# Optimization experiments

Measured on AMD Instinct MI355X. Metric: run time of the kernel, lower is better.

## Reference

```python
import jax, jax.numpy as jnp
import numpy as np

EPS = 1e-6

def _phi(x):
    # ELU + 1 feature map: strictly positive
    return jax.nn.elu(x) + 1.0

def setup_inputs() -> dict:
    key = jax.random.key(0)
    kq, kk, kv = jax.random.split(key, 3)
    B, T, H, D = 4, 8192, 16, 64
    q = jax.random.normal(kq, (B, T, H, D), dtype=jnp.float32)
    k = jax.random.normal(kk, (B, T, H, D), dtype=jnp.float32)
    v = jax.random.normal(kv, (B, T, H, D), dtype=jnp.float32)
    return {"q": q, "k": k, "v": v}

def _linear_attention(q, k, v):
    # q,k,v: [B,T,H,D] -> out [B,T,H,D]
    phi_q = _phi(q)
    phi_k = _phi(k)
    # time-major for scan: [T,B,H,D]
    pq = jnp.moveaxis(phi_q, 1, 0)
    pk = jnp.moveaxis(phi_k, 1, 0)
    vv = jnp.moveaxis(v, 1, 0)
    B, H, D = pq.shape[1], pq.shape[2], pq.shape[3]
    S0 = jnp.zeros((B, H, D, D), dtype=q.dtype)
    z0 = jnp.zeros((B, H, D), dtype=q.dtype)

    def step(carry, inp):
        S, z = carry
        q_t, k_t, v_t = inp  # each [B,H,D]
        S = S + k_t[..., :, None] * v_t[..., None, :]  # [B,H,D,D]
        z = z + k_t
        num = jnp.einsum('bhd,bhde->bhe', q_t, S)
        den = jnp.einsum('bhd,bhd->bh', q_t, z) + EPS
        return (S, z), num / den[..., None]

    _, out = jax.lax.scan(step, (S0, z0), (pq, pk, vv))
    return jnp.moveaxis(out, 0, 1)  # [B,T,H,D]

def reference(q, k, v):
    return _linear_attention(q, k, v)
```

## Files before the change

kernel.cpp:

```cpp
#include <hip/hip_runtime.h>
#include <hip/hip_bf16.h>


#define EPS_ 1e-6f

constexpr int Bc  = 4;
constexpr int Tc  = 8192;
constexpr int Hc  = 16;
constexpr int Dc  = 64;
constexpr int CH  = 128;
constexpr int NCH = Tc / CH;
constexpr int BHc = Bc * Hc;
constexpr int REC = Dc * Dc + Dc;
constexpr int SEG = 16;
constexpr int CPS = NCH / SEG;

typedef short  bf16x8 __attribute__((ext_vector_type(8)));
typedef float  f32x4  __attribute__((ext_vector_type(4)));

__device__ __forceinline__ float phi_f(float x) {
    return x > 0.f ? x + 1.f : __expf(x);
}
__device__ __forceinline__ unsigned short f2b(float x) {
    __hip_bfloat16 b = __float2bfloat16(x);
    return __builtin_bit_cast(unsigned short, b);
}
__device__ __forceinline__ float b2f(unsigned short u) {
    return __uint_as_float(((unsigned)u) << 16);
}
__device__ __forceinline__ int swz(int row, int colu) {
    return row * 136 + (colu ^ (((row >> 2) & 7) << 3));
}

__global__ __launch_bounds__(256, 4) void k_chunkscan(const float* __restrict__ kin,
                                                      const float* __restrict__ vin,
                                                      float* __restrict__ ws) {
    const int blk = blockIdx.x;
    const int bh  = blk >> 4, seg = blk & (SEG - 1);
    const int b   = bh >> 4,  h   = bh & 15;
    const int tid = threadIdx.x;
    const int w = tid >> 6, lane = tid & 63;
    const int l15 = lane & 15, quad = lane >> 4;

    __shared__ unsigned short ktr[64 * 136];
    __shared__ unsigned short vtr[64 * 136];
    __shared__ float zred[16][68];

    const int c0 = (tid & 15) << 2;
    const int rl = (tid >> 4) << 2;

    f32x4 acc[4];
    #pragma unroll
    for (int nt = 0; nt < 4; nt++) acc[nt] = (f32x4){0.f, 0.f, 0.f, 0.f};
    float zrun = 0.f;

    unsigned short hk[2][4][4], hv[2][4][4];
    float zp[4];

    auto load_chunk = [&](int c) {
        zp[0] = zp[1] = zp[2] = zp[3] = 0.f;
        #pragma unroll
        for (int sh = 0; sh < 2; ++sh) {
            const int r0 = rl + sh * 64;
            #pragma unroll
            for (int jj = 0; jj < 4; ++jj) {
                const size_t g = ((((size_t)b * Tc) + (c * CH + r0 + jj)) * Hc + h) * Dc + c0;
                const float4 kk = *(const float4*)(kin + g);
                const float4 vv = *(const float4*)(vin + g);
                hk[sh][jj][0] = f2b(phi_f(kk.x)); hk[sh][jj][1] = f2b(phi_f(kk.y));
                hk[sh][jj][2] = f2b(phi_f(kk.z)); hk[sh][jj][3] = f2b(phi_f(kk.w));
                hv[sh][jj][0] = f2b(vv.x); hv[sh][jj][1] = f2b(vv.y);
                hv[sh][jj][2] = f2b(vv.z); hv[sh][jj][3] = f2b(vv.w);
                #pragma unroll
                for (int j = 0; j < 4; ++j) zp[j] += b2f(hk[sh][jj][j]);
            }
        }
    };

    load_chunk(seg * CPS);

    for (int i = 0; i < CPS; ++i) {
        const int c = seg * CPS + i;
        float* rec = ws + (size_t)(bh * NCH + c) * REC;

        __syncthreads();

        #pragma unroll
        for (int sh = 0; sh < 2; ++sh) {
            const int r0 = rl + sh * 64;
            #pragma unroll
            for (int j = 0; j < 4; ++j) {
                *(ushort4*)&ktr[swz(c0 + j, r0)] =
                    make_ushort4(hk[sh][0][j], hk[sh][1][j], hk[sh][2][j], hk[sh][3][j]);
                *(ushort4*)&vtr[swz(c0 + j, r0)] =
                    make_ushort4(hv[sh][0][j], hv[sh][1][j], hv[sh][2][j], hv[sh][3][j]);
            }
        }
        #pragma unroll
        for (int j = 0; j < 4; ++j) zred[tid >> 4][c0 + j] = zp[j];

        if (i > 0) {
            #pragma unroll
            for (int nt = 0; nt < 4; nt++)
                #pragma unroll
                for (int r = 0; r < 4; r++)
                    rec[(16 * w + quad * 4 + r) * 64 + 16 * nt + l15] = acc[nt][r];
        }
        __syncthreads();

        float zs = 0.f;
        if (tid < 64) {
            if (i > 0) rec[4096 + tid] = zrun;
            #pragma unroll
            for (int g = 0; g < 16; g++) zs += zred[g][tid];
        }

        if (i + 1 < CPS) load_chunk(c + 1);

        #pragma unroll
        for (int ks = 0; ks < 4; ks++) {
            bf16x8 a = *(const bf16x8*)&vtr[swz(16 * w + l15, quad * 8 + ks * 32)];
            #pragma unroll
            for (int nt = 0; nt < 4; nt++) {
                bf16x8 bb = *(const bf16x8*)&ktr[swz(16 * nt + l15, quad * 8 + ks * 32)];
                acc[nt] = __builtin_amdgcn_mfma_f32_16x16x32_bf16(a, bb, acc[nt], 0, 0, 0);
            }
        }
        if (tid < 64) zrun += zs;
    }

    {
        float* rec0 = ws + (size_t)(bh * NCH + seg * CPS) * REC;
        #pragma unroll
        for (int nt = 0; nt < 4; nt++)
            #pragma unroll
            for (int r = 0; r < 4; r++)
                rec0[(16 * w + quad * 4 + r) * 64 + 16 * nt + l15] = acc[nt][r];
        if (tid < 64) rec0[4096 + tid] = zrun;
    }
}

__global__ __launch_bounds__(256) void k_segscan(float* __restrict__ ws) {
    const int bh = blockIdx.x;
    const int e  = blockIdx.y * 256 + threadIdx.x;
    if (e >= REC) return;
    float* p = ws + (size_t)bh * NCH * REC + e;
    float t[SEG];
    #pragma unroll
    for (int s = 0; s < SEG; ++s) t[s] = p[(size_t)(s * CPS) * REC];
    float run = 0.f;
    #pragma unroll
    for (int s = 0; s < SEG; ++s) { p[(size_t)(s * CPS) * REC] = run; run += t[s]; }
}

__global__ __launch_bounds__(512, 4) void k_output(const float* __restrict__ qin,
                                                   const float* __restrict__ kin,
                                                   const float* __restrict__ vin,
                                                   const float* __restrict__ ws,
                                                   float* __restrict__ outp) {
    const int chunk = blockIdx.x;
    const int bh = chunk >> 6, c = chunk & (NCH - 1);
    const int b = bh >> 4, h = bh & 15;
    const int t0 = c * CH;
    const int tid = threadIdx.x;
    const int w = tid >> 6, lane = tid & 63;
    const int l15 = lane & 15, quad = lane >> 4;

    __shared__ unsigned short qb[128][72];
    __shared__ unsigned short kb[128][72];
    __shared__ unsigned short sb[64][72];
    __shared__ unsigned short vb[64 * 136];
    __shared__ float zsh[64];
    __shared__ float den[128];

    {
        const int row = tid >> 2, cb = (tid & 3) << 4;
        const size_t g = ((((size_t)b * Tc) + (t0 + row)) * Hc + h) * Dc + cb;
        const float4* qp = (const float4*)(qin + g);
        const float4* kp = (const float4*)(kin + g);
        #pragma unroll
        for (int i = 0; i < 4; i++) {
            float4 qq = qp[i];
            float4 kk = kp[i];
            *(ushort4*)&qb[row][cb + 4 * i] =
                make_ushort4(f2b(phi_f(qq.x)), f2b(phi_f(qq.y)), f2b(phi_f(qq.z)), f2b(phi_f(qq.w)));
            *(ushort4*)&kb[row][cb + 4 * i] =
                make_ushort4(f2b(phi_f(kk.x)), f2b(phi_f(kk.y)), f2b(phi_f(kk.z)), f2b(phi_f(kk.w)));
        }
    }
    {
        const int c0 = (tid & 15) << 2;
        const int r0 = (tid >> 4) << 2;
        unsigned short hv[4][4];
        #pragma unroll
        for (int jj = 0; jj < 4; ++jj) {
            const size_t g = ((((size_t)b * Tc) + (t0 + r0 + jj)) * Hc + h) * Dc + c0;
            const float4 vv = *(const float4*)(vin + g);
            hv[jj][0] = f2b(vv.x); hv[jj][1] = f2b(vv.y);
            hv[jj][2] = f2b(vv.z); hv[jj][3] = f2b(vv.w);
        }
        #pragma unroll
        for (int j = 0; j < 4; ++j)
            *(ushort4*)&vb[swz(c0 + j, r0)] = make_ushort4(hv[0][j], hv[1][j], hv[2][j], hv[3][j]);
    }
    {
        const float* rec = ws + (size_t)chunk * REC;
        const float* bse = ws + (size_t)(bh * NCH + (c & ~(CPS - 1))) * REC;
        const bool cz = ((c & (CPS - 1)) == 0);
        #pragma unroll
        for (int i = 0; i < 2; i++) {
            const int idx = tid + i * 512;
            float4 sv = ((const float4*)rec)[idx];
            float4 bv = ((const float4*)bse)[idx];
            float4 t;
            if (cz) t = bv;
            else { t.x = sv.x + bv.x; t.y = sv.y + bv.y; t.z = sv.z + bv.z; t.w = sv.w + bv.w; }
            const int flat = idx * 4, e = flat >> 6, d = flat & 63;
            *(ushort4*)&sb[e][d] = make_ushort4(f2b(t.x), f2b(t.y), f2b(t.z), f2b(t.w));
        }
        if (tid < 16) {
            float4 zv = ((const float4*)(rec + 4096))[tid];
            float4 bz = ((const float4*)(bse + 4096))[tid];
            float4 t;
            if (cz) t = bz;
            else { t.x = zv.x + bz.x; t.y = zv.y + bz.y; t.z = zv.z + bz.z; t.w = zv.w + bz.w; }
            zsh[tid * 4 + 0] = t.x; zsh[tid * 4 + 1] = t.y;
            zsh[tid * 4 + 2] = t.z; zsh[tid * 4 + 3] = t.w;
        }
    }
    __syncthreads();

    if (tid < 128) {
        float s = 0.f;
        #pragma unroll
        for (int j = 0; j < 8; j++) {
            bf16x8 qv = *(const bf16x8*)&qb[tid][j * 8];
            #pragma unroll
            for (int u = 0; u < 8; u++) s += b2f((unsigned short)qv[u]) * zsh[j * 8 + u];
        }
        den[tid] = s + EPS_;
    }

    f32x4 acc[4];
    #pragma unroll
    for (int nt = 0; nt < 4; nt++) acc[nt] = (f32x4){0.f, 0.f, 0.f, 0.f};
    #pragma unroll
    for (int ks = 0; ks < 2; ks++) {
        bf16x8 a = *(const bf16x8*)&qb[16 * w + l15][quad * 8 + ks * 32];
        #pragma unroll
        for (int nt = 0; nt < 4; nt++) {
            bf16x8 bb = *(const bf16x8*)&sb[16 * nt + l15][quad * 8 + ks * 32];
            acc[nt] = __builtin_amdgcn_mfma_f32_16x16x32_bf16(a, bb, acc[nt], 0, 0, 0);
        }
    }

    f32x4 wt[8];
    #pragma unroll
    for (int nt = 0; nt < 8; nt++) wt[nt] = (f32x4){0.f, 0.f, 0.f, 0.f};
    #pragma unroll
    for (int ks = 0; ks < 2; ks++) {
        bf16x8 a = *(const bf16x8*)&qb[16 * w + l15][quad * 8 + ks * 32];
        #pragma unroll
        for (int nt = 0; nt < 4; nt++) {
            bf16x8 bb = *(const bf16x8*)&kb[16 * nt + l15][quad * 8 + ks * 32];
            wt[nt] = __builtin_amdgcn_mfma_f32_16x16x32_bf16(a, bb, wt[nt], 0, 0, 0);
        }
        if (w >= 4) {
            #pragma unroll
            for (int nt = 4; nt < 8; nt++) {
                bf16x8 bb = *(const bf16x8*)&kb[16 * nt + l15][quad * 8 + ks * 32];
                wt[nt] = __builtin_amdgcn_mfma_f32_16x16x32_bf16(a, bb, wt[nt], 0, 0, 0);
            }
        }
    }
    __syncthreads();

    {
        const int tbase = 16 * w + quad * 4;
        float rsum[4] = {0.f, 0.f, 0.f, 0.f};
        #pragma unroll
        for (int nt = 0; nt < 4; nt++) {
            const int s = 16 * nt + l15;
            #pragma unroll
            for (int r = 0; r < 4; r++) {
                float val = (s > tbase + r) ? 0.f : wt[nt][r];
                unsigned short wb16 = f2b(val);
                kb[tbase + r][s] = wb16;
                rsum[r] += b2f(wb16);
            }
        }
        if (w >= 4) {
            #pragma unroll
            for (int nt = 4; nt < 8; nt++) {
                const int s = 16 * nt + l15;
                #pragma unroll
                for (int r = 0; r < 4; r++) {
                    float val = (s > tbase + r) ? 0.f : wt[nt][r];
                    unsigned short wb16 = f2b(val);
                    qb[tbase + r][s - 64] = wb16;
                    rsum[r] += b2f(wb16);
                }
            }
        }
        #pragma unroll
        for (int r = 0; r < 4; r++) {
            float rs = rsum[r];
            rs += __shfl_xor(rs, 8, 16);
            rs += __shfl_xor(rs, 4, 16);
            rs += __shfl_xor(rs, 2, 16);
            rs += __shfl_xor(rs, 1, 16);
            if (l15 == 0) den[tbase + r] += rs;
        }
    }
    __syncthreads();

    #pragma unroll
    for (int ks = 0; ks < 2; ks++) {
        bf16x8 a = *(const bf16x8*)&kb[16 * w + l15][quad * 8 + ks * 32];
        #pragma unroll
        for (int nt = 0; nt < 4; nt++) {
            bf16x8 bb = *(const bf16x8*)&vb[swz(16 * nt + l15, quad * 8 + ks * 32)];
            acc[nt] = __builtin_amdgcn_mfma_f32_16x16x32_bf16(a, bb, acc[nt], 0, 0, 0);
        }
    }
    if (w >= 4) {
        #pragma unroll
        for (int ks = 2; ks < 4; ks++) {
            bf16x8 a = *(const bf16x8*)&qb[16 * w + l15][quad * 8 + (ks - 2) * 32];
            #pragma unroll
            for (int nt = 0; nt < 4; nt++) {
                bf16x8 bb = *(const bf16x8*)&vb[swz(16 * nt + l15, quad * 8 + ks * 32)];
                acc[nt] = __builtin_amdgcn_mfma_f32_16x16x32_bf16(a, bb, acc[nt], 0, 0, 0);
            }
        }
    }

    #pragma unroll
    for (int r = 0; r < 4; r++) {
        const int t = 16 * w + quad * 4 + r;
        const float inv = 1.0f / den[t];
        const size_t gbase = ((((size_t)b * Tc) + (t0 + t)) * Hc + h) * Dc;
        #pragma unroll
        for (int nt = 0; nt < 4; nt++) {
            outp[gbase + 16 * nt + l15] = acc[nt][r] * inv;
        }
    }
}

extern "C" void kernel_launch(void* const* d_in, const int* in_sizes, int n_in,
                              void* d_out, int out_size, void* d_ws, size_t ws_size,
                              hipStream_t stream) {
    const float* q = (const float*)d_in[0];
    const float* k = (const float*)d_in[1];
    const float* v = (const float*)d_in[2];
    float* out = (float*)d_out;
    float* ws  = (float*)d_ws;

    k_chunkscan<<<BHc * SEG, 256, 0, stream>>>(k, v, ws);
    dim3 g2(BHc, (REC + 255) / 256);
    k_segscan<<<g2, 256, 0, stream>>>(ws);
    k_output<<<BHc * NCH, 512, 0, stream>>>(q, k, v, ws, out);
}
```

Measured before the change: 507.6 us.

## Shrink k_output LDS with XOR-swizzled unpadded tiles and buffer aliasing

Replaces the padded shared-memory tiles in the output kernel with unpadded XOR-swizzled layouts. The S-state buffer and the transposed V tile now share one buffer: V is held in registers and written into the same space after the S products finish, behind the existing barrier. This cuts LDS per block so more blocks can be resident, and the launch-bounds minimum is raised from 4 to 6 blocks. In exchange, V stays live in registers longer, and the tighter register budget may cause spills.

```diff
diff --git a/kernel.cpp b/kernel.cpp
--- a/kernel.cpp
+++ b/kernel.cpp
@@ -28,8 +28,14 @@
 __device__ __forceinline__ float b2f(unsigned short u) {
     return __uint_as_float(((unsigned)u) << 16);
 }
-__device__ __forceinline__ int swz(int row, int colu) {
+__device__ __forceinline__ int swz136(int row, int colu) {
     return row * 136 + (colu ^ (((row >> 2) & 7) << 3));
+}
+__device__ __forceinline__ int swz64(int row, int colu) {
+    return row * 64 + (colu ^ ((row & 7) << 3));
+}
+__device__ __forceinline__ int swz128(int row, int colu) {
+    return row * 128 + (colu ^ ((row & 15) << 3));
 }
 
 __global__ __launch_bounds__(256, 4) void k_chunkscan(const float* __restrict__ kin,
@@ -90,9 +96,9 @@
             const int r0 = rl + sh * 64;
             #pragma unroll
             for (int j = 0; j < 4; ++j) {
-                *(ushort4*)&ktr[swz(c0 + j, r0)] =
+                *(ushort4*)&ktr[swz136(c0 + j, r0)] =
                     make_ushort4(hk[sh][0][j], hk[sh][1][j], hk[sh][2][j], hk[sh][3][j]);
-                *(ushort4*)&vtr[swz(c0 + j, r0)] =
+                *(ushort4*)&vtr[swz136(c0 + j, r0)] =
                     make_ushort4(hv[sh][0][j], hv[sh][1][j], hv[sh][2][j], hv[sh][3][j]);
             }
         }
@@ -119,10 +125,10 @@
 
         #pragma unroll
         for (int ks = 0; ks < 4; ks++) {
-            bf16x8 a = *(const bf16x8*)&vtr[swz(16 * w + l15, quad * 8 + ks * 32)];
+            bf16x8 a = *(const bf16x8*)&vtr[swz136(16 * w + l15, quad * 8 + ks * 32)];
             #pragma unroll
             for (int nt = 0; nt < 4; nt++) {
-                bf16x8 bb = *(const bf16x8*)&ktr[swz(16 * nt + l15, quad * 8 + ks * 32)];
+                bf16x8 bb = *(const bf16x8*)&ktr[swz136(16 * nt + l15, quad * 8 + ks * 32)];
                 acc[nt] = __builtin_amdgcn_mfma_f32_16x16x32_bf16(a, bb, acc[nt], 0, 0, 0);
             }
         }
@@ -153,7 +159,7 @@
     for (int s = 0; s < SEG; ++s) { p[(size_t)(s * CPS) * REC] = run; run += t[s]; }
 }
 
-__global__ __launch_bounds__(512, 4) void k_output(const float* __restrict__ qin,
+__global__ __launch_bounds__(512, 6) void k_output(const float* __restrict__ qin,
                                                    const float* __restrict__ kin,
                                                    const float* __restrict__ vin,
                                                    const float* __restrict__ ws,
@@ -166,10 +172,9 @@
     const int w = tid >> 6, lane = tid & 63;
     const int l15 = lane & 15, quad = lane >> 4;
 
-    __shared__ unsigned short qb[128][72];
-    __shared__ unsigned short kb[128][72];
-    __shared__ unsigned short sb[64][72];
-    __shared__ unsigned short vb[64 * 136];
+    __shared__ unsigned short qb[128 * 64];
+    __shared__ unsigned short kb[128 * 64];
+    __shared__ unsigned short ub[64 * 128];
     __shared__ float zsh[64];
     __shared__ float den[128];
 
@@ -182,26 +187,23 @@
         for (int i = 0; i < 4; i++) {
             float4 qq = qp[i];
             float4 kk = kp[i];
-            *(ushort4*)&qb[row][cb + 4 * i] =
+            *(ushort4*)&qb[swz64(row, cb + 4 * i)] =
                 make_ushort4(f2b(phi_f(qq.x)), f2b(phi_f(qq.y)), f2b(phi_f(qq.z)), f2b(phi_f(qq.w)));
-            *(ushort4*)&kb[row][cb + 4 * i] =
+            *(ushort4*)&kb[swz64(row, cb + 4 * i)] =
                 make_ushort4(f2b(phi_f(kk.x)), f2b(phi_f(kk.y)), f2b(phi_f(kk.z)), f2b(phi_f(kk.w)));
         }
     }
-    {
-        const int c0 = (tid & 15) << 2;
-        const int r0 = (tid >> 4) << 2;
-        unsigned short hv[4][4];
+    unsigned short hv[4][4];
+    const int vc0 = (tid & 15) << 2;
+    const int vr0 = (tid >> 4) << 2;
+    {
         #pragma unroll
         for (int jj = 0; jj < 4; ++jj) {
-            const size_t g = ((((size_t)b * Tc) + (t0 + r0 + jj)) * Hc + h) * Dc + c0;
+            const size_t g = ((((size_t)b * Tc) + (t0 + vr0 + jj)) * Hc + h) * Dc + vc0;
             const float4 vv = *(const float4*)(vin + g);
             hv[jj][0] = f2b(vv.x); hv[jj][1] = f2b(vv.y);
             hv[jj][2] = f2b(vv.z); hv[jj][3] = f2b(vv.w);
         }
-        #pragma unroll
-        for (int j = 0; j < 4; ++j)
-            *(ushort4*)&vb[swz(c0 + j, r0)] = make_ushort4(hv[0][j], hv[1][j], hv[2][j], hv[3][j]);
     }
     {
         const float* rec = ws + (size_t)chunk * REC;
@@ -216,7 +218,7 @@
             if (cz) t = bv;
             else { t.x = sv.x + bv.x; t.y = sv.y + bv.y; t.z = sv.z + bv.z; t.w = sv.w + bv.w; }
             const int flat = idx * 4, e = flat >> 6, d = flat & 63;
-            *(ushort4*)&sb[e][d] = make_ushort4(f2b(t.x), f2b(t.y), f2b(t.z), f2b(t.w));
+            *(ushort4*)&ub[swz64(e, d)] = make_ushort4(f2b(t.x), f2b(t.y), f2b(t.z), f2b(t.w));
         }
         if (tid < 16) {
             float4 zv = ((const float4*)(rec + 4096))[tid];
@@ -234,7 +236,7 @@
         float s = 0.f;
         #pragma unroll
         for (int j = 0; j < 8; j++) {
-            bf16x8 qv = *(const bf16x8*)&qb[tid][j * 8];
+            bf16x8 qv = *(const bf16x8*)&qb[swz64(tid, j * 8)];
             #pragma unroll
             for (int u = 0; u < 8; u++) s += b2f((unsigned short)qv[u]) * zsh[j * 8 + u];
         }
@@ -246,10 +248,10 @@
     for (int nt = 0; nt < 4; nt++) acc[nt] = (f32x4){0.f, 0.f, 0.f, 0.f};
     #pragma unroll
     for (int ks = 0; ks < 2; ks++) {
-        bf16x8 a = *(const bf16x8*)&qb[16 * w + l15][quad * 8 + ks * 32];
-        #pragma unroll
-        for (int nt = 0; nt < 4; nt++) {
-            bf16x8 bb = *(const bf16x8*)&sb[16 * nt + l15][quad * 8 + ks * 32];
+        bf16x8 a = *(const bf16x8*)&qb[swz64(16 * w + l15, quad * 8 + ks * 32)];
+        #pragma unroll
+        for (int nt = 0; nt < 4; nt++) {
+            bf16x8 bb = *(const bf16x8*)&ub[swz64(16 * nt + l15, quad * 8 + ks * 32)];
             acc[nt] = __builtin_amdgcn_mfma_f32_16x16x32_bf16(a, bb, acc[nt], 0, 0, 0);
         }
     }
@@ -259,22 +261,28 @@
     for (int nt = 0; nt < 8; nt++) wt[nt] = (f32x4){0.f, 0.f, 0.f, 0.f};
     #pragma unroll
     for (int ks = 0; ks < 2; ks++) {
-        bf16x8 a = *(const bf16x8*)&qb[16 * w + l15][quad * 8 + ks * 32];
-        #pragma unroll
-        for (int nt = 0; nt < 4; nt++) {
-            bf16x8 bb = *(const bf16x8*)&kb[16 * nt + l15][quad * 8 + ks * 32];
+        bf16x8 a = *(const bf16x8*)&qb[swz64(16 * w + l15, quad * 8 + ks * 32)];
+        #pragma unroll
+        for (int nt = 0; nt < 4; nt++) {
+            bf16x8 bb = *(const bf16x8*)&kb[swz64(16 * nt + l15, quad * 8 + ks * 32)];
             wt[nt] = __builtin_amdgcn_mfma_f32_16x16x32_bf16(a, bb, wt[nt], 0, 0, 0);
         }
         if (w >= 4) {
             #pragma unroll
             for (int nt = 4; nt < 8; nt++) {
-                bf16x8 bb = *(const bf16x8*)&kb[16 * nt + l15][quad * 8 + ks * 32];
+                bf16x8 bb = *(const bf16x8*)&kb[swz64(16 * nt + l15, quad * 8 + ks * 32)];
                 wt[nt] = __builtin_amdgcn_mfma_f32_16x16x32_bf16(a, bb, wt[nt], 0, 0, 0);
             }
         }
     }
     __syncthreads();
 
+    {
+        #pragma unroll
+        for (int j = 0; j < 4; ++j)
+            *(ushort4*)&ub[swz128(vc0 + j, vr0)] =
+                make_ushort4(hv[0][j], hv[1][j], hv[2][j], hv[3][j]);
+    }
     {
         const int tbase = 16 * w + quad * 4;
         float rsum[4] = {0.f, 0.f, 0.f, 0.f};
@@ -285,7 +293,7 @@
             for (int r = 0; r < 4; r++) {
                 float val = (s > tbase + r) ? 0.f : wt[nt][r];
                 unsigned short wb16 = f2b(val);
-                kb[tbase + r][s] = wb16;
+                kb[swz64(tbase + r, s)] = wb16;
                 rsum[r] += b2f(wb16);
             }
         }
@@ -297,7 +305,7 @@
                 for (int r = 0; r < 4; r++) {
                     float val = (s > tbase + r) ? 0.f : wt[nt][r];
                     unsigned short wb16 = f2b(val);
-                    qb[tbase + r][s - 64] = wb16;
+                    qb[swz64(tbase + r, s - 64)] = wb16;
                     rsum[r] += b2f(wb16);
                 }
             }
@@ -316,20 +324,20 @@
 
     #pragma unroll
     for (int ks = 0; ks < 2; ks++) {
-        bf16x8 a = *(const bf16x8*)&kb[16 * w + l15][quad * 8 + ks * 32];
-        #pragma unroll
-        for (int nt = 0; nt < 4; nt++) {
-            bf16x8 bb = *(const bf16x8*)&vb[swz(16 * nt + l15, quad * 8 + ks * 32)];
+        bf16x8 a = *(const bf16x8*)&kb[swz64(16 * w + l15, quad * 8 + ks * 32)];
+        #pragma unroll
+        for (int nt = 0; nt < 4; nt++) {
+            bf16x8 bb = *(const bf16x8*)&ub[swz128(16 * nt + l15, quad * 8 + ks * 32)];
             acc[nt] = __builtin_amdgcn_mfma_f32_16x16x32_bf16(a, bb, acc[nt], 0, 0, 0);
         }
     }
     if (w >= 4) {
         #pragma unroll
         for (int ks = 2; ks < 4; ks++) {
-            bf16x8 a = *(const bf16x8*)&qb[16 * w + l15][quad * 8 + (ks - 2) * 32];
+            bf16x8 a = *(const bf16x8*)&qb[swz64(16 * w + l15, quad * 8 + (ks - 2) * 32)];
             #pragma unroll
             for (int nt = 0; nt < 4; nt++) {
-                bf16x8 bb = *(const bf16x8*)&vb[swz(16 * nt + l15, quad * 8 + ks * 32)];
+                bf16x8 bb = *(const bf16x8*)&ub[swz128(16 * nt + l15, quad * 8 + ks * 32)];
                 acc[nt] = __builtin_amdgcn_mfma_f32_16x16x32_bf16(a, bb, acc[nt], 0, 0, 0);
             }
         }
```

Result: no change. 513.3 us (+1.1%).
